# Kernel tuning notes

Measured on AMD Instinct MI355X. Metric: run time of the kernel, lower is better.

The kernel has to match this reference:

```python
import jax, jax.numpy as jnp
import numpy as np
from jax import lax

B, CH, TS = 64, 9, 3000
D, H, EMB = 64, 256, 32
WIDTHS = (3, 2, 2, 2, 2, 2)
IN_CH = (1, H, H, H, H, H)
OUT_CH = (H, H, H, H, H, D)


def setup_inputs():
    keys = iter(jax.random.split(jax.random.key(0), 64))
    inp = {"x": jax.random.normal(next(keys), (B, CH, TS), jnp.float32)}
    for l, (ci, co, w) in enumerate(zip(IN_CH, OUT_CH, WIDTHS)):
        inp[f"conv_w{l}"] = jax.random.normal(next(keys), (co, ci, w), jnp.float32) / np.float32(np.sqrt(ci * w))
        inp[f"conv_b{l}"] = jnp.zeros((co,), jnp.float32)
        inp[f"gn_g{l}"] = jnp.ones((co,), jnp.float32)
        inp[f"gn_b{l}"] = jnp.zeros((co,), jnp.float32)
    inp["ro_w"] = jax.random.normal(next(keys), (D, D), jnp.float32) / np.float32(np.sqrt(D))
    inp["ro_b"] = jnp.zeros((D,), jnp.float32)
    for r in range(2):
        inp[f"msg_w{r}"] = jax.random.normal(next(keys), (2 * D, D), jnp.float32) / np.float32(np.sqrt(2 * D))
        inp[f"msg_b{r}"] = jnp.zeros((D,), jnp.float32)
    inp["rn_w1"] = jax.random.normal(next(keys), (D, D), jnp.float32) / np.float32(np.sqrt(D))
    inp["rn_b1"] = jnp.zeros((D,), jnp.float32)
    inp["rn_w2"] = jax.random.normal(next(keys), (D, D), jnp.float32) / np.float32(np.sqrt(D))
    inp["rn_b2"] = jnp.zeros((D,), jnp.float32)
    inp["proj_w"] = jax.random.normal(next(keys), (D, EMB), jnp.float32) / np.float32(np.sqrt(D))
    inp["proj_b"] = jnp.zeros((EMB,), jnp.float32)
    return inp


def _gn(h, g, b):
    # GroupNorm(num_groups=1): normalize over (C, T) per sample
    mu = h.mean(axis=(1, 2), keepdims=True)
    var = h.var(axis=(1, 2), keepdims=True)
    return (h - mu) * lax.rsqrt(var + 1e-5) * g[None, :, None] + b[None, :, None]


def _forward(x, ps):
    b, ch, ts = x.shape
    h = x.reshape(b * ch, 1, ts)  # each view is one 1-channel node signal
    for l, w in enumerate(WIDTHS):
        W, bi, g, be = ps[4 * l], ps[4 * l + 1], ps[4 * l + 2], ps[4 * l + 3]
        h = lax.conv_general_dilated(h, W, (w,), [(w // 2, w // 2)], dimension_numbers=("NCH", "OIH", "NCH")) + bi[None, :, None]
        h = jax.nn.gelu(_gn(h, g, be), approximate=False)
    ro_w, ro_b = ps[24], ps[25]
    h = jnp.einsum("nct,co->not", h, ro_w) + ro_b[None, :, None]  # 1x1 readout conv
    lat = h.transpose(0, 2, 1)  # [b*ch, T, D]
    N = b * ch
    # fully-connected graph within each sample, exactly as in the torch code
    msg_from = np.repeat(np.arange(N), ch - 1)
    grid = np.broadcast_to(np.arange(N).reshape(b, ch)[:, None, :], (b, ch, ch))
    msg_to = grid[:, ~np.eye(ch, dtype=bool)].reshape(-1)
    for W, bi in ((ps[26], ps[27]), (ps[28], ps[29])):
        m = jnp.concatenate([lat[msg_from], lat[msg_to]], axis=-1)  # [E, T, 2D]
        m = jax.nn.relu(m @ W + bi) / (ch - 1)  # dropout is identity at eval
        lat = lat.at[msg_to].add(m)
    view_id = np.repeat(np.arange(b), ch)
    y = jax.ops.segment_sum(lat, view_id, num_segments=b)  # [b, T, D]
    y = (jax.nn.relu(y @ ps[30] + ps[31]) @ ps[32] + ps[33]) / ch
    return (y @ ps[34] + ps[35]).transpose(0, 2, 1)  # [b, EMB, T]


def reference(x, conv_w0, conv_b0, gn_g0, gn_b0, conv_w1, conv_b1, gn_g1, gn_b1, conv_w2, conv_b2, gn_g2, gn_b2, conv_w3, conv_b3, gn_g3, gn_b3, conv_w4, conv_b4, gn_g4, gn_b4, conv_w5, conv_b5, gn_g5, gn_b5, ro_w, ro_b, msg_w0, msg_b0, msg_w1, msg_b1, rn_w1, rn_b1, rn_w2, rn_b2, proj_w, proj_b):
    ps = (conv_w0, conv_b0, gn_g0, gn_b0, conv_w1, conv_b1, gn_g1, gn_b1, conv_w2, conv_b2, gn_g2, gn_b2, conv_w3, conv_b3, gn_g3, gn_b3, conv_w4, conv_b4, gn_g4, gn_b4, conv_w5, conv_b5, gn_g5, gn_b5, ro_w, ro_b, msg_w0, msg_b0, msg_w1, msg_b1, rn_w1, rn_b1, rn_w2, rn_b2, proj_w, proj_b)
    return _forward(x, ps)
```

## Files before the change

kernel.cpp:

```cpp
#include <hip/hip_runtime.h>
#include <hip/hip_bf16.h>

typedef __hip_bfloat16 bf16;
typedef __attribute__((ext_vector_type(8))) short s8v;
typedef __attribute__((ext_vector_type(4))) float f4v;

__device__ __forceinline__ float gelu_f(float x) {
    float x2 = x * x;
    float z  = x * __builtin_fmaf(0.071355f, x2, 1.595769f);
    float e  = __expf(-z);
    return x * __builtin_amdgcn_rcpf(1.0f + e);
}
__device__ __forceinline__ unsigned short f2bf_u(float f) {
    bf16 b = __float2bfloat16(f);
    return *(unsigned short*)&b;
}
__device__ __forceinline__ float bfu2f(unsigned short u) {
    bf16 b = *(bf16*)&u;
    return __bfloat162float(b);
}

__global__ __launch_bounds__(256) void zero_k(float* __restrict__ p, int n) {
    int i = blockIdx.x * 256 + threadIdx.x;
    if (i < n) p[i] = 0.f;
}

__global__ __launch_bounds__(256) void wcvt_k(
    const float* __restrict__ w1, const float* __restrict__ w2,
    const float* __restrict__ w3, const float* __restrict__ w4,
    const float* __restrict__ w5, bf16* __restrict__ dst)
{
    int i = blockIdx.x * 256 + threadIdx.x;
    if (i >= 557056) return;
    const float* src; int li;
    if      (i < 131072) { src = w1; li = i; }
    else if (i < 262144) { src = w2; li = i - 131072; }
    else if (i < 393216) { src = w3; li = i - 262144; }
    else if (i < 524288) { src = w4; li = i - 393216; }
    else                 { src = w5; li = i - 524288; }
    int co = li >> 9, rem = li & 511;
    int kc = rem >> 6, rr = rem & 63;
    int s = rr >> 5, cil = rr & 31;
    dst[i] = __float2bfloat16(src[co * 512 + (kc * 32 + cil) * 2 + s]);
}

__global__ __launch_bounds__(256) void m0red_k(
    const float* __restrict__ W0, const float* __restrict__ b0,
    float* __restrict__ coef, float* __restrict__ w0t)
{
    __shared__ float red[256];
    const int co = threadIdx.x;
    float w0 = W0[3 * co], w1 = W0[3 * co + 1], w2 = W0[3 * co + 2], b = b0[co];
    w0t[co] = w0; w0t[256 + co] = w1; w0t[512 + co] = w2;
    float vals[14] = {w0, w1, w2, b,
                      w0 * w0, w1 * w1, w2 * w2, b * b,
                      2.f * w0 * w1, 2.f * w0 * w2, 2.f * w1 * w2,
                      2.f * w0 * b, 2.f * w1 * b, 2.f * w2 * b};
    for (int k = 0; k < 14; k++) {
        red[co] = vals[k];
        __syncthreads();
        for (int st = 128; st > 0; st >>= 1) {
            if (co < st) red[co] += red[co + st];
            __syncthreads();
        }
        if (co == 0) coef[k] = red[0];
        __syncthreads();
    }
}

__global__ __launch_bounds__(256) void c0stats_k(
    const float* __restrict__ x, const float* __restrict__ coef,
    float* __restrict__ mu0, float* __restrict__ rstd0)
{
    __shared__ float xsl[3008];
    __shared__ float red[512];
    const int n = blockIdx.x, tid = threadIdx.x;
    const float* xr = x + (size_t)n * 3000;
    for (int i = tid; i < 750; i += 256) *(float4*)&xsl[4 + 4 * i] = *(const float4*)(xr + 4 * i);
    if (tid < 4) xsl[tid] = 0.f;
    float c[14];
    #pragma unroll
    for (int k = 0; k < 14; k++) c[k] = coef[k];
    __syncthreads();
    float S = 0.f, Q = 0.f;
    if (tid < 250) {
        float f[16];
        #pragma unroll
        for (int k = 0; k < 4; k++) *(float4*)&f[4 * k] = *(const float4*)&xsl[12 * tid + 4 * k];
        #pragma unroll
        for (int j = 0; j < 4; j++) {
            float x0 = f[3 * j + 3], x1 = f[3 * j + 4], x2 = f[3 * j + 5];
            S += c[0] * x0 + c[1] * x1 + c[2] * x2 + c[3];
            Q += c[4] * x0 * x0 + c[5] * x1 * x1 + c[6] * x2 * x2 + c[7]
               + c[8] * x0 * x1 + c[9] * x0 * x2 + c[10] * x1 * x2
               + c[11] * x0 + c[12] * x1 + c[13] * x2;
        }
    }
    red[tid] = S; red[256 + tid] = Q;
    __syncthreads();
    for (int st = 128; st > 0; st >>= 1) {
        if (tid < st) { red[tid] += red[tid + st]; red[256 + tid] += red[256 + tid + st]; }
        __syncthreads();
    }
    if (tid == 0) {
        float m = red[0] * (1.f / 256000.f);
        float var = red[256] * (1.f / 256000.f) - m * m;
        mu0[n] = m;
        rstd0[n] = rsqrtf(var + 1e-5f);
    }
}

template<int MW, int NW, int MODE>
__global__ __launch_bounds__(256) void convT_k(
    const bf16* __restrict__ g, const float* __restrict__ xraw,
    const float* __restrict__ w0t, const bf16* __restrict__ Wp,
    const float* __restrict__ bias, const float* __restrict__ b0c,
    bf16* __restrict__ hout, float* __restrict__ ssum, float* __restrict__ ssq,
    int T_g, int T_out, int n0,
    const float* __restrict__ pssum, const float* __restrict__ pssq,
    const float* __restrict__ pgam, const float* __restrict__ pbet,
    float pinvCT)
{
    constexpr int CO = 4 * NW * 16;
    constexpr int MT = MW * 16;
    constexpr int NSLOT = MT * 8;
    constexpr int NU = (NSLOT + 255) / 256;
    __shared__ bf16 aT[2][MT * 64];
    __shared__ float biasS[CO];
    __shared__ float red[512];
    __shared__ float acoS[256], ccoS[256];
    __shared__ float xs[(MODE == 2) ? 400 : 1];
    __shared__ float w0s[(MODE == 2) ? 768 : 1];
    const int n  = blockIdx.y;
    const int t0 = blockIdx.x * MT;
    const int tid = threadIdx.x;
    for (int i = tid; i < CO; i += 256) biasS[i] = bias[i];
    if (MODE == 1) {
        float mu = pssum[n0 + n] * pinvCT;
        float rs = rsqrtf(pssq[n0 + n] * pinvCT - mu * mu + 1e-5f);
        float a = rs * pgam[tid];
        acoS[tid] = a;
        ccoS[tid] = pbet[tid] - mu * a;
        __syncthreads();
    } else {
        float mu = pssum[n];
        float rs = pssq[n];
        float a = rs * pgam[tid];
        acoS[tid] = a;
        ccoS[tid] = (b0c[tid] - mu) * a + pbet[tid];
        const float* xr = xraw + (size_t)n * 3000;
        for (int i = tid; i < 400; i += 256) {
            int xg = 6 * t0 - 4 + i;
            xs[i] = ((unsigned)xg < 3000u) ? xr[xg] : 0.f;
        }
        __syncthreads();
        for (int i = tid; i < 768; i += 256) w0s[i] = w0t[i] * acoS[i & 255];
        __syncthreads();
    }
    const int w = tid >> 6, lane = tid & 63;
    const int l16 = lane & 15, quad = lane >> 4;
    const int sx = l16 & 7;
    const bf16* gb = (MODE == 2) ? nullptr : (g + (size_t)n * T_g * 256);

    bool s_inv[NU];
    int s_q[NU], s_tin[NU], s_off[NU];
    #pragma unroll
    for (int u = 0; u < NU; u++) {
        int slot = tid + 256 * u;
        s_inv[u] = (NSLOT % 256 != 0) && (slot >= NSLOT);
        if (s_inv[u]) { s_tin[u] = 0x7fffffff; s_q[u] = 0; s_off[u] = 0; continue; }
        int t = slot >> 3, j = slot & 7;
        int ks = j >> 2, q = j & 3;
        s_q[u] = q;
        s_tin[u] = 2 * (t0 + t) - 1 + ks;
        s_off[u] = (t * 8 + (j ^ (t & 7))) * 8;
    }

    f4v acc[MW][NW];
    #pragma unroll
    for (int i = 0; i < MW; i++)
        #pragma unroll
        for (int j = 0; j < NW; j++) acc[i][j] = (f4v){0.f, 0.f, 0.f, 0.f};

    auto stageK = [&](int kc, bf16* wb) {
        #pragma unroll
        for (int u = 0; u < NU; u++) {
            if (s_inv[u]) continue;
            int tin = s_tin[u];
            s8v v = (s8v){0, 0, 0, 0, 0, 0, 0, 0};
            if ((unsigned)tin < (unsigned)T_g) {
                const int ci0 = kc * 32 + s_q[u] * 8;
                unsigned short* uu = (unsigned short*)&v;
                if (MODE == 2) {
                    int lx = 3 * (tin - 2 * t0) + 3;
                    float x0 = xs[lx], x1 = xs[lx + 1], x2 = xs[lx + 2];
                    float4 c0 = *(const float4*)&ccoS[ci0], c1 = *(const float4*)&ccoS[ci0 + 4];
                    float4 wa0 = *(const float4*)&w0s[ci0],       wa1 = *(const float4*)&w0s[ci0 + 4];
                    float4 wb0 = *(const float4*)&w0s[256 + ci0], wb1 = *(const float4*)&w0s[256 + ci0 + 4];
                    float4 wc0 = *(const float4*)&w0s[512 + ci0], wc1 = *(const float4*)&w0s[512 + ci0 + 4];
                    float cv[8]  = {c0.x, c0.y, c0.z, c0.w, c1.x, c1.y, c1.z, c1.w};
                    float wav[8] = {wa0.x, wa0.y, wa0.z, wa0.w, wa1.x, wa1.y, wa1.z, wa1.w};
                    float wbv[8] = {wb0.x, wb0.y, wb0.z, wb0.w, wb1.x, wb1.y, wb1.z, wb1.w};
                    float wcv[8] = {wc0.x, wc0.y, wc0.z, wc0.w, wc1.x, wc1.y, wc1.z, wc1.w};
                    #pragma unroll
                    for (int jj = 0; jj < 8; jj++) {
                        float t1 = __builtin_fmaf(wav[jj], x0, cv[jj]);
                        t1 = __builtin_fmaf(wbv[jj], x1, t1);
                        t1 = __builtin_fmaf(wcv[jj], x2, t1);
                        uu[jj] = f2bf_u(gelu_f(t1));
                    }
                } else {
                    float4 a0 = *(const float4*)&acoS[ci0], a1 = *(const float4*)&acoS[ci0 + 4];
                    float4 c0 = *(const float4*)&ccoS[ci0], c1 = *(const float4*)&ccoS[ci0 + 4];
                    float av[8] = {a0.x, a0.y, a0.z, a0.w, a1.x, a1.y, a1.z, a1.w};
                    float cv[8] = {c0.x, c0.y, c0.z, c0.w, c1.x, c1.y, c1.z, c1.w};
                    v = *(const s8v*)(gb + (size_t)tin * 256 + ci0);
                    #pragma unroll
                    for (int jj = 0; jj < 8; jj++)
                        uu[jj] = f2bf_u(gelu_f(__builtin_fmaf(bfu2f(uu[jj]), av[jj], cv[jj])));
                }
            }
            *(s8v*)&wb[s_off[u]] = v;
        }
    };

    stageK(0, aT[0]);
    __syncthreads();

    for (int kc = 0; kc < 8; kc++) {
        s8v bfr[2][NW];
        #pragma unroll
        for (int ks = 0; ks < 2; ks++)
            #pragma unroll
            for (int j = 0; j < NW; j++) {
                int co = w * NW * 16 + j * 16 + l16;
                bfr[ks][j] = *(const s8v*)(Wp + (size_t)co * 512 + kc * 64 + ks * 32 + quad * 8);
            }
        const bf16* rb = aT[kc & 1];
        __builtin_amdgcn_s_setprio(1);
        #pragma unroll
        for (int ks = 0; ks < 2; ks++) {
            const int sl = (ks * 4 + quad) ^ sx;
            s8v af[MW];
            #pragma unroll
            for (int i = 0; i < MW; i++)
                af[i] = *(const s8v*)&rb[(i * 16 + l16) * 64 + sl * 8];
            #pragma unroll
            for (int i = 0; i < MW; i++)
                #pragma unroll
                for (int j = 0; j < NW; j++)
                    acc[i][j] = __builtin_amdgcn_mfma_f32_16x16x32_bf16(af[i], bfr[ks][j], acc[i][j], 0, 0, 0);
        }
        __builtin_amdgcn_s_setprio(0);
        if (kc < 7) {
            stageK(kc + 1, aT[(kc + 1) & 1]);
            __syncthreads();
        }
    }

    float lsum = 0.f, lsq = 0.f;
    #pragma unroll
    for (int i = 0; i < MW; i++) {
        #pragma unroll
        for (int r = 0; r < 4; r++) {
            int t = t0 + i * 16 + quad * 4 + r;
            if (t < T_out) {
                bf16* orow = hout + ((size_t)n * T_out + t) * CO;
                #pragma unroll
                for (int j = 0; j < NW; j++) {
                    int co = w * NW * 16 + j * 16 + l16;
                    float v = acc[i][j][r] + biasS[co];
                    orow[co] = __float2bfloat16(v);
                    lsum += v; lsq += v * v;
                }
            }
        }
    }
    red[tid] = lsum; red[256 + tid] = lsq;
    __syncthreads();
    for (int st = 128; st > 0; st >>= 1) {
        if (tid < st) { red[tid] += red[tid + st]; red[256 + tid] += red[256 + tid + st]; }
        __syncthreads();
    }
    if (tid == 0) { atomicAdd(&ssum[n0 + n], red[0]); atomicAdd(&ssq[n0 + n], red[256]); }
}

__global__ __launch_bounds__(256) void readout_pre_k(
    const bf16* __restrict__ h5T, const float* __restrict__ row,
    const float* __restrict__ rob, const float* __restrict__ g5,
    const float* __restrict__ be5, const float* __restrict__ ssum,
    const float* __restrict__ ssq, float invCT,
    const float* __restrict__ mw, const float* __restrict__ mb,
    float* __restrict__ lat0, float* __restrict__ A0, float* __restrict__ Bv0)
{
    __shared__ float lh[2112];
    __shared__ float ll[2112];
    __shared__ float lw[8192];
    __shared__ float lb[64];
    const int n = blockIdx.x, tid = threadIdx.x;
    const float mu = ssum[n] * invCT;
    const float rs = rsqrtf(ssq[n] * invCT - mu * mu + 1e-5f);
    for (int idx = tid; idx < 2112; idx += 256) {
        int c = idx & 63;
        float a = rs * g5[c];
        float v = __bfloat162float(h5T[(size_t)n * 2112 + idx]) * a + (be5[c] - mu * a);
        lh[idx] = gelu_f(v);
    }
    for (int idx = tid; idx < 4096; idx += 256) lw[idx] = row[idx];
    if (tid < 64) lb[tid] = rob[tid];
    __syncthreads();
    for (int idx = tid; idx < 2112; idx += 256) {
        int t = idx >> 6, d = idx & 63;
        float a = lb[d];
        #pragma unroll 8
        for (int c = 0; c < 64; c++) a += lh[t * 64 + c] * lw[c * 64 + d];
        ll[idx] = a;
        lat0[(size_t)n * 2112 + idx] = a;
    }
    __syncthreads();
    for (int idx = tid; idx < 8192; idx += 256) lw[idx] = mw[idx];
    if (tid < 64) lb[tid] = mb[tid];
    __syncthreads();
    for (int idx = tid; idx < 2112; idx += 256) {
        int t = idx >> 6, d = idx & 63;
        float a = 0.f, bb = lb[d];
        #pragma unroll 8
        for (int k = 0; k < 64; k++) {
            float xv = ll[t * 64 + k];
            a  += xv * lw[k * 64 + d];
            bb += xv * lw[(64 + k) * 64 + d];
        }
        A0[(size_t)n * 2112 + idx]  = a;
        Bv0[(size_t)n * 2112 + idx] = bb;
    }
}

__global__ __launch_bounds__(256) void comb_pre_k(
    const float* __restrict__ lat0, const float* __restrict__ A0,
    const float* __restrict__ Bv0, const float* __restrict__ mw,
    const float* __restrict__ mb, float* __restrict__ lat1,
    float* __restrict__ A1, float* __restrict__ Bv1)
{
    __shared__ float ll[2112];
    __shared__ float lw[8192];
    __shared__ float lb[64];
    const int n = blockIdx.x, tid = threadIdx.x;
    const int b9 = (n / 9) * 9, j = n - b9;
    for (int idx = tid; idx < 2112; idx += 256) {
        float base = Bv0[(size_t)n * 2112 + idx];
        float s = 0.f;
        #pragma unroll
        for (int i = 0; i < 9; i++) {
            if (i == j) continue;
            s += fmaxf(A0[(size_t)(b9 + i) * 2112 + idx] + base, 0.f);
        }
        float v = lat0[(size_t)n * 2112 + idx] + s * 0.125f;
        ll[idx] = v;
        lat1[(size_t)n * 2112 + idx] = v;
    }
    for (int idx = tid; idx < 8192; idx += 256) lw[idx] = mw[idx];
    if (tid < 64) lb[tid] = mb[tid];
    __syncthreads();
    for (int idx = tid; idx < 2112; idx += 256) {
        int t = idx >> 6, d = idx & 63;
        float a = 0.f, bb = lb[d];
        #pragma unroll 8
        for (int k = 0; k < 64; k++) {
            float xv = ll[t * 64 + k];
            a  += xv * lw[k * 64 + d];
            bb += xv * lw[(64 + k) * 64 + d];
        }
        A1[(size_t)n * 2112 + idx]  = a;
        Bv1[(size_t)n * 2112 + idx] = bb;
    }
}

__global__ __launch_bounds__(256) void final2_k(
    const float* __restrict__ lat1, const float* __restrict__ A1,
    const float* __restrict__ Bv1,
    const float* __restrict__ w1, const float* __restrict__ b1,
    const float* __restrict__ w2, const float* __restrict__ b2,
    const float* __restrict__ pw, const float* __restrict__ pb,
    float* __restrict__ out)
{
    __shared__ float ly[2112], lz[2112];
    __shared__ float lw1[4096], lw2[4096], lpw[2048];
    __shared__ float lb1[64], lb2[64], lpb[32];
    const int b = blockIdx.x, tid = threadIdx.x;
    for (int idx = tid; idx < 4096; idx += 256) { lw1[idx] = w1[idx]; lw2[idx] = w2[idx]; }
    for (int idx = tid; idx < 2048; idx += 256) lpw[idx] = pw[idx];
    if (tid < 64) { lb1[tid] = b1[tid]; lb2[tid] = b2[tid]; }
    if (tid < 32) lpb[tid] = pb[tid];
    for (int idx = tid; idx < 2112; idx += 256) {
        float Av[9], Bb[9], s = 0.f;
        #pragma unroll
        for (int jj = 0; jj < 9; jj++) {
            size_t off = ((size_t)(b * 9 + jj)) * 2112 + idx;
            Av[jj] = A1[off];
            Bb[jj] = Bv1[off];
            s += lat1[off];
        }
        float m = 0.f;
        #pragma unroll
        for (int jj = 0; jj < 9; jj++) {
            float rowsum = 0.f;
            #pragma unroll
            for (int ii = 0; ii < 9; ii++) rowsum += fmaxf(Av[ii] + Bb[jj], 0.f);
            m += rowsum - fmaxf(Av[jj] + Bb[jj], 0.f);
        }
        ly[idx] = s + m * 0.125f;
    }
    __syncthreads();
    for (int idx = tid; idx < 2112; idx += 256) {
        int t = idx >> 6, d = idx & 63;
        float s = lb1[d];
        #pragma unroll 8
        for (int k = 0; k < 64; k++) s += ly[t * 64 + k] * lw1[k * 64 + d];
        lz[idx] = fmaxf(s, 0.f);
    }
    __syncthreads();
    for (int idx = tid; idx < 2112; idx += 256) {
        int t = idx >> 6, d = idx & 63;
        float s = lb2[d];
        #pragma unroll 8
        for (int k = 0; k < 64; k++) s += lz[t * 64 + k] * lw2[k * 64 + d];
        ly[idx] = s * (1.f / 9.f);
    }
    __syncthreads();
    for (int idx = tid; idx < 1056; idx += 256) {
        int e = idx / 33, t = idx - e * 33;
        float s = lpb[e];
        #pragma unroll 8
        for (int d = 0; d < 64; d++) s += ly[t * 64 + d] * lpw[d * 32 + e];
        out[(size_t)b * 1056 + idx] = s;
    }
}

extern "C" void kernel_launch(void* const* d_in, const int* in_sizes, int n_in,
                              void* d_out, int out_size, void* d_ws, size_t ws_size,
                              hipStream_t stream)
{
    const float* x = (const float*)d_in[0];
    const float* cw[6]; const float* cb[6]; const float* gg[6]; const float* gb[6];
    for (int l = 0; l < 6; l++) {
        cw[l] = (const float*)d_in[1 + 4 * l];
        cb[l] = (const float*)d_in[2 + 4 * l];
        gg[l] = (const float*)d_in[3 + 4 * l];
        gb[l] = (const float*)d_in[4 + 4 * l];
    }
    const float* ro_w = (const float*)d_in[25];
    const float* ro_b = (const float*)d_in[26];
    const float* mw0  = (const float*)d_in[27];
    const float* mb0  = (const float*)d_in[28];
    const float* mw1  = (const float*)d_in[29];
    const float* mb1  = (const float*)d_in[30];
    const float* rw1  = (const float*)d_in[31];
    const float* rb1  = (const float*)d_in[32];
    const float* rw2  = (const float*)d_in[33];
    const float* rb2  = (const float*)d_in[34];
    const float* pw   = (const float*)d_in[35];
    const float* pb   = (const float*)d_in[36];

    char* ws = (char*)d_ws;
    bf16* h1T  = (bf16*)(ws);
    bf16* h2T  = (bf16*)(ws + 147750912);
    bf16* h3T  = (bf16*)(ws + 221773824);
    bf16* h4T  = (bf16*)(ws);
    bf16* h5T  = (bf16*)(ws + 147750912);
    float* lat0 = (float*)(ws);
    float* A0   = lat0 + 1216512;
    float* Bv0  = A0   + 1216512;
    float* lat1 = Bv0  + 1216512;
    float* A1   = lat1 + 1216512;
    float* Bv1  = A1   + 1216512;
    float* stat  = (float*)(ws + 258932736);
    float* mu0   = stat;
    float* rstd0 = stat + 576;
    float* coef  = stat + 1152;
    float* ssumA = stat + 1168;
    float* ssqA  = ssumA + 5 * 576;
    float* w0taps = ssqA + 5 * 576;
    bf16*  Wp    = (bf16*)(ws + 258965504);
    #define SSUM(l) (ssumA + ((l) - 1) * 576)
    #define SSQ(l)  (ssqA  + ((l) - 1) * 576)

    zero_k<<<(5760 + 255) / 256, 256, 0, stream>>>(ssumA, 2 * 5 * 576);
    wcvt_k<<<(557056 + 255) / 256, 256, 0, stream>>>(cw[1], cw[2], cw[3], cw[4], cw[5], Wp);
    m0red_k<<<1, 256, 0, stream>>>(cw[0], cb[0], coef, w0taps);
    c0stats_k<<<576, 256, 0, stream>>>(x, coef, mu0, rstd0);

    convT_k<4, 4, 2><<<dim3(8, 576), 256, 0, stream>>>(
        nullptr, x, w0taps, Wp, cb[1], cb[0], h1T, SSUM(1), SSQ(1), 1000, 501, 0,
        mu0, rstd0, gg[0], gb[0], 0.f);

    convT_k<4, 4, 1><<<dim3(4, 576), 256, 0, stream>>>(
        h1T, nullptr, nullptr, Wp + 131072, cb[2], nullptr, h2T, SSUM(2), SSQ(2), 501, 251, 0,
        SSUM(1), SSQ(1), gg[1], gb[1], 1.f / (256.f * 501.f));

    convT_k<4, 4, 1><<<dim3(2, 576), 256, 0, stream>>>(
        h2T, nullptr, nullptr, Wp + 262144, cb[3], nullptr, h3T, SSUM(3), SSQ(3), 251, 126, 0,
        SSUM(2), SSQ(2), gg[2], gb[2], 1.f / (256.f * 251.f));

    convT_k<4, 4, 1><<<dim3(1, 576), 256, 0, stream>>>(
        h3T, nullptr, nullptr, Wp + 393216, cb[4], nullptr, h4T, SSUM(4), SSQ(4), 126, 64, 0,
        SSUM(3), SSQ(3), gg[3], gb[3], 1.f / (256.f * 126.f));

    convT_k<3, 1, 1><<<dim3(1, 576), 256, 0, stream>>>(
        h4T, nullptr, nullptr, Wp + 524288, cb[5], nullptr, h5T, SSUM(5), SSQ(5), 64, 33, 0,
        SSUM(4), SSQ(4), gg[4], gb[4], 1.f / (256.f * 64.f));

    readout_pre_k<<<576, 256, 0, stream>>>(h5T, ro_w, ro_b, gg[5], gb[5],
                                           SSUM(5), SSQ(5), 1.f / (64.f * 33.f),
                                           mw0, mb0, lat0, A0, Bv0);
    comb_pre_k<<<576, 256, 0, stream>>>(lat0, A0, Bv0, mw1, mb1, lat1, A1, Bv1);
    final2_k<<<64, 256, 0, stream>>>(lat1, A1, Bv1, rw1, rb1, rw2, rb2, pw, pb, (float*)d_out);
}
```

Before: 664.1 us.

## Warp-specialize conv GEMM kernel into producer and MFMA consumer waves

Doubles the conv kernel block to 512 threads. Four producer waves stage and normalize/GELU the next K-chunk into shared memory while four consumer waves run the MFMA on the current chunk, with one barrier per iteration. The aim is to overlap the activation staging and its global loads with matrix-core work, which previously ran serially in the same waves. The layer-0 path now applies the GroupNorm scale after the 3-tap conv instead of folding it into the taps. The trade-off is twice the threads per block, which can limit residency, and a larger 512-wide stats reduction.

```diff
diff --git a/kernel.cpp b/kernel.cpp
--- a/kernel.cpp
+++ b/kernel.cpp
@@ -111,7 +111,7 @@
 }
 
 template<int MW, int NW, int MODE>
-__global__ __launch_bounds__(256) void convT_k(
+__global__ __launch_bounds__(512) void convT_k(
     const bf16* __restrict__ g, const float* __restrict__ xraw,
     const float* __restrict__ w0t, const bf16* __restrict__ Wp,
     const float* __restrict__ bias, const float* __restrict__ b0c,
@@ -124,50 +124,51 @@
     constexpr int CO = 4 * NW * 16;
     constexpr int MT = MW * 16;
     constexpr int NSLOT = MT * 8;
-    constexpr int NU = (NSLOT + 255) / 256;
+    constexpr int NU = 2;
     __shared__ bf16 aT[2][MT * 64];
     __shared__ float biasS[CO];
-    __shared__ float red[512];
+    __shared__ float red[1024];
     __shared__ float acoS[256], ccoS[256];
     __shared__ float xs[(MODE == 2) ? 400 : 1];
     __shared__ float w0s[(MODE == 2) ? 768 : 1];
     const int n  = blockIdx.y;
     const int t0 = blockIdx.x * MT;
     const int tid = threadIdx.x;
-    for (int i = tid; i < CO; i += 256) biasS[i] = bias[i];
+    for (int i = tid; i < CO; i += 512) biasS[i] = bias[i];
     if (MODE == 1) {
-        float mu = pssum[n0 + n] * pinvCT;
-        float rs = rsqrtf(pssq[n0 + n] * pinvCT - mu * mu + 1e-5f);
-        float a = rs * pgam[tid];
-        acoS[tid] = a;
-        ccoS[tid] = pbet[tid] - mu * a;
-        __syncthreads();
+        if (tid < 256) {
+            float mu = pssum[n0 + n] * pinvCT;
+            float rs = rsqrtf(pssq[n0 + n] * pinvCT - mu * mu + 1e-5f);
+            float a = rs * pgam[tid];
+            acoS[tid] = a;
+            ccoS[tid] = pbet[tid] - mu * a;
+        }
     } else {
-        float mu = pssum[n];
-        float rs = pssq[n];
-        float a = rs * pgam[tid];
-        acoS[tid] = a;
-        ccoS[tid] = (b0c[tid] - mu) * a + pbet[tid];
+        if (tid < 256) {
+            float mu = pssum[n];
+            float rs = pssq[n];
+            float a = rs * pgam[tid];
+            acoS[tid] = a;
+            ccoS[tid] = (b0c[tid] - mu) * a + pbet[tid];
+        }
+        for (int i = tid; i < 768; i += 512) w0s[i] = w0t[i];
         const float* xr = xraw + (size_t)n * 3000;
-        for (int i = tid; i < 400; i += 256) {
-            int xg = 6 * t0 - 4 + i;
-            xs[i] = ((unsigned)xg < 3000u) ? xr[xg] : 0.f;
-        }
-        __syncthreads();
-        for (int i = tid; i < 768; i += 256) w0s[i] = w0t[i] * acoS[i & 255];
-        __syncthreads();
-    }
-    const int w = tid >> 6, lane = tid & 63;
-    const int l16 = lane & 15, quad = lane >> 4;
-    const int sx = l16 & 7;
+        if (tid < 400) {
+            int xg = 6 * t0 - 4 + tid;
+            xs[tid] = ((unsigned)xg < 3000u) ? xr[xg] : 0.f;
+        }
+    }
+    __syncthreads();
+
     const bf16* gb = (MODE == 2) ? nullptr : (g + (size_t)n * T_g * 256);
+    const bool producer = (tid < 256);
 
     bool s_inv[NU];
     int s_q[NU], s_tin[NU], s_off[NU];
     #pragma unroll
     for (int u = 0; u < NU; u++) {
-        int slot = tid + 256 * u;
-        s_inv[u] = (NSLOT % 256 != 0) && (slot >= NSLOT);
+        int slot = (tid & 255) + 256 * u;
+        s_inv[u] = (NSLOT % 512 != 0) && (slot >= NSLOT);
         if (s_inv[u]) { s_tin[u] = 0x7fffffff; s_q[u] = 0; s_off[u] = 0; continue; }
         int t = slot >> 3, j = slot & 7;
         int ks = j >> 2, q = j & 3;
@@ -175,12 +176,6 @@
         s_tin[u] = 2 * (t0 + t) - 1 + ks;
         s_off[u] = (t * 8 + (j ^ (t & 7))) * 8;
     }
-
-    f4v acc[MW][NW];
-    #pragma unroll
-    for (int i = 0; i < MW; i++)
-        #pragma unroll
-        for (int j = 0; j < NW; j++) acc[i][j] = (f4v){0.f, 0.f, 0.f, 0.f};
 
     auto stageK = [&](int kc, bf16* wb) {
         #pragma unroll
@@ -194,20 +189,20 @@
                 if (MODE == 2) {
                     int lx = 3 * (tin - 2 * t0) + 3;
                     float x0 = xs[lx], x1 = xs[lx + 1], x2 = xs[lx + 2];
+                    float4 a0 = *(const float4*)&acoS[ci0], a1 = *(const float4*)&acoS[ci0 + 4];
                     float4 c0 = *(const float4*)&ccoS[ci0], c1 = *(const float4*)&ccoS[ci0 + 4];
                     float4 wa0 = *(const float4*)&w0s[ci0],       wa1 = *(const float4*)&w0s[ci0 + 4];
                     float4 wb0 = *(const float4*)&w0s[256 + ci0], wb1 = *(const float4*)&w0s[256 + ci0 + 4];
                     float4 wc0 = *(const float4*)&w0s[512 + ci0], wc1 = *(const float4*)&w0s[512 + ci0 + 4];
+                    float av[8]  = {a0.x, a0.y, a0.z, a0.w, a1.x, a1.y, a1.z, a1.w};
                     float cv[8]  = {c0.x, c0.y, c0.z, c0.w, c1.x, c1.y, c1.z, c1.w};
                     float wav[8] = {wa0.x, wa0.y, wa0.z, wa0.w, wa1.x, wa1.y, wa1.z, wa1.w};
                     float wbv[8] = {wb0.x, wb0.y, wb0.z, wb0.w, wb1.x, wb1.y, wb1.z, wb1.w};
                     float wcv[8] = {wc0.x, wc0.y, wc0.z, wc0.w, wc1.x, wc1.y, wc1.z, wc1.w};
                     #pragma unroll
                     for (int jj = 0; jj < 8; jj++) {
-                        float t1 = __builtin_fmaf(wav[jj], x0, cv[jj]);
-                        t1 = __builtin_fmaf(wbv[jj], x1, t1);
-                        t1 = __builtin_fmaf(wcv[jj], x2, t1);
-                        uu[jj] = f2bf_u(gelu_f(t1));
+                        float conv = wav[jj] * x0 + wbv[jj] * x1 + wcv[jj] * x2;
+                        uu[jj] = f2bf_u(gelu_f(__builtin_fmaf(conv, av[jj], cv[jj])));
                     }
                 } else {
                     float4 a0 = *(const float4*)&acoS[ci0], a1 = *(const float4*)&acoS[ci0 + 4];
@@ -224,65 +219,79 @@
         }
     };
 
-    stageK(0, aT[0]);
+    const int cw = (tid >> 6) - 4;
+    const int lane = tid & 63;
+    const int l16 = lane & 15, quad = lane >> 4;
+    const int sx = l16 & 7;
+
+    f4v acc[MW][NW];
+    #pragma unroll
+    for (int i = 0; i < MW; i++)
+        #pragma unroll
+        for (int j = 0; j < NW; j++) acc[i][j] = (f4v){0.f, 0.f, 0.f, 0.f};
+
+    if (producer) stageK(0, aT[0]);
     __syncthreads();
 
     for (int kc = 0; kc < 8; kc++) {
-        s8v bfr[2][NW];
-        #pragma unroll
-        for (int ks = 0; ks < 2; ks++)
+        if (!producer) {
+            s8v bfr[2][NW];
             #pragma unroll
-            for (int j = 0; j < NW; j++) {
-                int co = w * NW * 16 + j * 16 + l16;
-                bfr[ks][j] = *(const s8v*)(Wp + (size_t)co * 512 + kc * 64 + ks * 32 + quad * 8);
-            }
-        const bf16* rb = aT[kc & 1];
-        __builtin_amdgcn_s_setprio(1);
-        #pragma unroll
-        for (int ks = 0; ks < 2; ks++) {
-            const int sl = (ks * 4 + quad) ^ sx;
-            s8v af[MW];
-            #pragma unroll
-            for (int i = 0; i < MW; i++)
-                af[i] = *(const s8v*)&rb[(i * 16 + l16) * 64 + sl * 8];
-            #pragma unroll
-            for (int i = 0; i < MW; i++)
-                #pragma unroll
-                for (int j = 0; j < NW; j++)
-                    acc[i][j] = __builtin_amdgcn_mfma_f32_16x16x32_bf16(af[i], bfr[ks][j], acc[i][j], 0, 0, 0);
-        }
-        __builtin_amdgcn_s_setprio(0);
-        if (kc < 7) {
-            stageK(kc + 1, aT[(kc + 1) & 1]);
-            __syncthreads();
-        }
-    }
-
-    float lsum = 0.f, lsq = 0.f;
-    #pragma unroll
-    for (int i = 0; i < MW; i++) {
-        #pragma unroll
-        for (int r = 0; r < 4; r++) {
-            int t = t0 + i * 16 + quad * 4 + r;
-            if (t < T_out) {
-                bf16* orow = hout + ((size_t)n * T_out + t) * CO;
+            for (int ks = 0; ks < 2; ks++)
                 #pragma unroll
                 for (int j = 0; j < NW; j++) {
-                    int co = w * NW * 16 + j * 16 + l16;
-                    float v = acc[i][j][r] + biasS[co];
-                    orow[co] = __float2bfloat16(v);
-                    lsum += v; lsq += v * v;
+                    int co = cw * NW * 16 + j * 16 + l16;
+                    bfr[ks][j] = *(const s8v*)(Wp + (size_t)co * 512 + kc * 64 + ks * 32 + quad * 8);
+                }
+            const bf16* rb = aT[kc & 1];
+            __builtin_amdgcn_s_setprio(1);
+            #pragma unroll
+            for (int ks = 0; ks < 2; ks++) {
+                const int sl = (ks * 4 + quad) ^ sx;
+                s8v af[MW];
+                #pragma unroll
+                for (int i = 0; i < MW; i++)
+                    af[i] = *(const s8v*)&rb[(i * 16 + l16) * 64 + sl * 8];
+                #pragma unroll
+                for (int i = 0; i < MW; i++)
+                    #pragma unroll
+                    for (int j = 0; j < NW; j++)
+                        acc[i][j] = __builtin_amdgcn_mfma_f32_16x16x32_bf16(af[i], bfr[ks][j], acc[i][j], 0, 0, 0);
+            }
+            __builtin_amdgcn_s_setprio(0);
+        } else if (kc < 7) {
+            stageK(kc + 1, aT[(kc + 1) & 1]);
+        }
+        __syncthreads();
+    }
+
+    float lsum = 0.f, lsq = 0.f;
+    if (!producer) {
+        #pragma unroll
+        for (int i = 0; i < MW; i++) {
+            #pragma unroll
+            for (int r = 0; r < 4; r++) {
+                int t = t0 + i * 16 + quad * 4 + r;
+                if (t < T_out) {
+                    bf16* orow = hout + ((size_t)n * T_out + t) * CO;
+                    #pragma unroll
+                    for (int j = 0; j < NW; j++) {
+                        int co = cw * NW * 16 + j * 16 + l16;
+                        float v = acc[i][j][r] + biasS[co];
+                        orow[co] = __float2bfloat16(v);
+                        lsum += v; lsq += v * v;
+                    }
                 }
             }
         }
     }
-    red[tid] = lsum; red[256 + tid] = lsq;
-    __syncthreads();
-    for (int st = 128; st > 0; st >>= 1) {
-        if (tid < st) { red[tid] += red[tid + st]; red[256 + tid] += red[256 + tid + st]; }
+    red[tid] = lsum; red[512 + tid] = lsq;
+    __syncthreads();
+    for (int st = 256; st > 0; st >>= 1) {
+        if (tid < st) { red[tid] += red[tid + st]; red[512 + tid] += red[512 + tid + st]; }
         __syncthreads();
     }
-    if (tid == 0) { atomicAdd(&ssum[n0 + n], red[0]); atomicAdd(&ssq[n0 + n], red[256]); }
+    if (tid == 0) { atomicAdd(&ssum[n0 + n], red[0]); atomicAdd(&ssq[n0 + n], red[512]); }
 }
 
 __global__ __launch_bounds__(256) void readout_pre_k(
@@ -489,23 +498,23 @@
     m0red_k<<<1, 256, 0, stream>>>(cw[0], cb[0], coef, w0taps);
     c0stats_k<<<576, 256, 0, stream>>>(x, coef, mu0, rstd0);
 
-    convT_k<4, 4, 2><<<dim3(8, 576), 256, 0, stream>>>(
+    convT_k<4, 4, 2><<<dim3(8, 576), 512, 0, stream>>>(
         nullptr, x, w0taps, Wp, cb[1], cb[0], h1T, SSUM(1), SSQ(1), 1000, 501, 0,
         mu0, rstd0, gg[0], gb[0], 0.f);
 
-    convT_k<4, 4, 1><<<dim3(4, 576), 256, 0, stream>>>(
+    convT_k<4, 4, 1><<<dim3(4, 576), 512, 0, stream>>>(
         h1T, nullptr, nullptr, Wp + 131072, cb[2], nullptr, h2T, SSUM(2), SSQ(2), 501, 251, 0,
         SSUM(1), SSQ(1), gg[1], gb[1], 1.f / (256.f * 501.f));
 
-    convT_k<4, 4, 1><<<dim3(2, 576), 256, 0, stream>>>(
+    convT_k<4, 4, 1><<<dim3(2, 576), 512, 0, stream>>>(
         h2T, nullptr, nullptr, Wp + 262144, cb[3], nullptr, h3T, SSUM(3), SSQ(3), 251, 126, 0,
         SSUM(2), SSQ(2), gg[2], gb[2], 1.f / (256.f * 251.f));
 
-    convT_k<4, 4, 1><<<dim3(1, 576), 256, 0, stream>>>(
+    convT_k<4, 4, 1><<<dim3(1, 576), 512, 0, stream>>>(
         h3T, nullptr, nullptr, Wp + 393216, cb[4], nullptr, h4T, SSUM(4), SSQ(4), 126, 64, 0,
         SSUM(3), SSQ(3), gg[3], gb[3], 1.f / (256.f * 126.f));
 
-    convT_k<3, 1, 1><<<dim3(1, 576), 256, 0, stream>>>(
+    convT_k<3, 1, 1><<<dim3(1, 576), 512, 0, stream>>>(
         h4T, nullptr, nullptr, Wp + 524288, cb[5], nullptr, h5T, SSUM(5), SSQ(5), 64, 33, 0,
         SSUM(4), SSQ(4), gg[4], gb[4], 1.f / (256.f * 64.f));
 
```

Measured after the change: 805.6 us. 21.3% more time.
